# Kernel tuning notes

Measured on AMD Instinct MI355X. Metric: run time of the kernel, lower is better.

## Reference

```python
import jax, jax.numpy as jnp
import numpy as np

B, L, E, H = 64, 256, 1024, 16
HD = E // H
ROPE_BASE = 10000.0


def rope(x):
    # x: [B, H, L, HD]; torchtune-style interleaved RoPE along the seq axis
    Lx, D = x.shape[2], x.shape[3]
    inv_freq = 1.0 / (ROPE_BASE ** (jnp.arange(0, D, 2, dtype=jnp.float32) / D))
    ang = jnp.arange(Lx, dtype=jnp.float32)[:, None] * inv_freq[None, :]  # [L, D/2]
    cos, sin = jnp.cos(ang), jnp.sin(ang)
    x0, x1 = x[..., 0::2], x[..., 1::2]
    r0 = x0 * cos - x1 * sin
    r1 = x1 * cos + x0 * sin
    return jnp.stack([r0, r1], axis=-1).reshape(x.shape)


def setup_inputs() -> dict:
    key = jax.random.key(0)
    ks = jax.random.split(key, 6)
    s = 0.02
    return {
        "x": jax.random.normal(ks[0], (B, L, E), jnp.float32),
        "Wq": jax.random.normal(ks[1], (E, E), jnp.float32) * s,
        "bq": jnp.zeros((E,), jnp.float32),
        "Wk": jax.random.normal(ks[2], (E, E), jnp.float32) * s,
        "bk": jnp.zeros((E,), jnp.float32),
        "Wv": jax.random.normal(ks[3], (E, E), jnp.float32) * s,
        "bv": jnp.zeros((E,), jnp.float32),
        "Wo": jax.random.normal(ks[4], (E, E), jnp.float32) * s,
        "bo": jnp.zeros((E,), jnp.float32),
        "attention_mask": jnp.ones((B, L), bool),
    }


def reference(x, Wq, bq, Wk, bk, Wv, bv, Wo, bo, attention_mask):
    Bq, Lq, _ = x.shape
    # QKV projections (nn.Linear: y = x @ W.T + b), split heads -> [B, H, L, HD]
    q = (x @ Wq.T + bq).reshape(Bq, Lq, H, HD).transpose(0, 2, 1, 3)
    k = (x @ Wk.T + bk).reshape(Bq, Lq, H, HD).transpose(0, 2, 1, 3)
    v = (x @ Wv.T + bv).reshape(Bq, Lq, H, HD).transpose(0, 2, 1, 3)
    q = rope(q)
    k = rope(k)
    # combined causal + padding mask: [B, 1, Lq, Lq]
    causal = jnp.tril(jnp.ones((Lq, Lq), bool))
    mask = causal[None, None, :, :] & attention_mask[:, None, None, :]
    scale = 1.0 / np.sqrt(HD).astype(np.float32)
    scores = jnp.einsum('bhqd,bhkd->bhqk', q, k) * scale
    scores = jnp.where(mask, scores, jnp.finfo(scores.dtype).min)
    attn = jax.nn.softmax(scores, axis=-1)
    out = jnp.einsum('bhqk,bhkd->bhqd', attn, v)
    out = out.transpose(0, 2, 1, 3).reshape(Bq, Lq, E)
    return out @ Wo.T + bo
```

## Files before the change

kernel.cpp:

```cpp
#include <hip/hip_runtime.h>
#include <hip/hip_bf16.h>

typedef __attribute__((ext_vector_type(4))) float f32x4;
typedef __attribute__((ext_vector_type(8))) short s16x8;
typedef unsigned short ushort_t;

__device__ __forceinline__ ushort_t f2bf(float f) {
    union { float f; unsigned u; } v; v.f = f;
    unsigned r = v.u + 0x7fffu + ((v.u >> 16) & 1u);
    return (ushort_t)(r >> 16);
}

__device__ __forceinline__ void gload16(const ushort_t* g, ushort_t* l) {
    __builtin_amdgcn_global_load_lds(
        (const __attribute__((address_space(1))) unsigned int*)g,
        (__attribute__((address_space(3))) unsigned int*)l,
        16, 0, 0);
}

#define BAR()  asm volatile("s_barrier" ::: "memory")
#define LGK0() do { asm volatile("s_waitcnt lgkmcnt(0)" ::: "memory"); __builtin_amdgcn_sched_barrier(0); } while (0)
#define VMC(n) asm volatile("s_waitcnt vmcnt(" #n ")" ::: "memory")

__global__ void cvt_bf16(const float* __restrict__ in, ushort_t* __restrict__ out, int n8) {
    int i = blockIdx.x * blockDim.x + threadIdx.x;
    if (i >= n8) return;
    const float4* p = (const float4*)in;
    float4 a = p[2 * i], b = p[2 * i + 1];
    s16x8 v;
    v[0] = (short)f2bf(a.x); v[1] = (short)f2bf(a.y);
    v[2] = (short)f2bf(a.z); v[3] = (short)f2bf(a.w);
    v[4] = (short)f2bf(b.x); v[5] = (short)f2bf(b.y);
    v[6] = (short)f2bf(b.z); v[7] = (short)f2bf(b.w);
    *(s16x8*)(out + (size_t)i * 8) = v;
}

__global__ void rope_tab_k(float* __restrict__ cosT, float* __restrict__ sinT) {
    int i = blockIdx.x * blockDim.x + threadIdx.x;
    int l = i >> 5, fi = i & 31;
    float inv = powf(10000.f, -2.f * (float)fi / 64.f);
    float ang = (float)l * inv;
    cosT[i] = cosf(ang);
    sinT[i] = sinf(ang);
}


__device__ __forceinline__ void stage32(const ushort_t* __restrict__ src,
                                        ushort_t* chunk, int tid, int kk) {
#pragma unroll
    for (int j = 0; j < 2; ++j) {
        int row = (tid >> 2) + j * 128;
        int gslot = (tid & 3) ^ ((row >> 1) & 3);
        gload16(src + (size_t)row * 1024 + kk + gslot * 8,
                chunk + (size_t)tid * 8 + (size_t)j * 4096);
    }
}

__device__ __forceinline__ s16x8 rdA32(const ushort_t* chunk, int wm, int m, int lane) {
    int row = wm * 128 + m * 16 + (lane & 15);
    int slot = (lane >> 4) ^ ((row >> 1) & 3);
    return *(const s16x8*)&chunk[row * 32 + (slot << 3)];
}
__device__ __forceinline__ s16x8 rdB32(const ushort_t* chunk, int wn, int n, int lane) {
    int row = wn * 64 + n * 16 + (lane & 15);
    int slot = (lane >> 4) ^ ((row >> 1) & 3);
    return *(const s16x8*)&chunk[row * 32 + (slot << 3)];
}

template <int MODE>
__global__ __launch_bounds__(512, 2) void gemm256(const ushort_t* __restrict__ A,
                                                  const ushort_t* __restrict__ Wt,
                                                  const float* __restrict__ bz0,
                                                  const float* __restrict__ bz1,
                                                  const float* __restrict__ bz2,
                                                  ushort_t* __restrict__ o0,
                                                  ushort_t* __restrict__ o1,
                                                  ushort_t* __restrict__ o2,
                                                  float* __restrict__ of,
                                                  const float* __restrict__ cosT,
                                                  const float* __restrict__ sinT,
                                                  int ntn) {
    __shared__ ushort_t lds[4][2][8192];

    const int nwg = 64 * ntn;
    const int orig = blockIdx.x;
    const int wg = (orig % 8) * (nwg / 8) + orig / 8;
    const int tn = wg % ntn, tm = wg / ntn;

    const int tid = threadIdx.x, lane = tid & 63, wid = tid >> 6;
    const int wm = wid >> 2, wn = wid & 3;

    f32x4 acc[8][4];
#pragma unroll
    for (int i = 0; i < 8; ++i)
#pragma unroll
        for (int j = 0; j < 4; ++j) acc[i][j] = (f32x4){0.f, 0.f, 0.f, 0.f};

    const ushort_t* Abase = A + (size_t)(tm * 256) * 1024;
    const ushort_t* Bbase = Wt + (size_t)(tn * 256) * 1024;

#pragma unroll
    for (int p = 0; p < 3; ++p) {
        stage32(Abase, &lds[p][0][0], tid, p * 32);
        stage32(Bbase, &lds[p][1][0], tid, p * 32);
    }

#pragma unroll 1
    for (int u = 0; u < 32; ++u) {
        const ushort_t* cA = &lds[u & 3][0][0];
        const ushort_t* cB = &lds[u & 3][1][0];
        ushort_t* sA = &lds[(u + 3) & 3][0][0];
        ushort_t* sB = &lds[(u + 3) & 3][1][0];
        const int kt = (u + 3 < 32 ? u + 3 : 31) * 32;
        s16x8 b_[4], a_[8];

        VMC(8);
        BAR();
        stage32(Abase, sA, tid, kt);
        stage32(Bbase, sB, tid, kt);
#pragma unroll
        for (int n = 0; n < 4; ++n) b_[n] = rdB32(cB, wn, n, lane);
#pragma unroll
        for (int m = 0; m < 8; ++m) a_[m] = rdA32(cA, wm, m, lane);
        LGK0();
        __builtin_amdgcn_s_setprio(1);
#pragma unroll
        for (int m = 0; m < 8; ++m)
#pragma unroll
            for (int n = 0; n < 4; ++n)
                acc[m][n] = __builtin_amdgcn_mfma_f32_16x16x32_bf16(a_[m], b_[n], acc[m][n], 0, 0, 0);
        __builtin_amdgcn_s_setprio(0);
    }
    VMC(0);

    const int rb0 = tm * 256 + wm * 128 + ((lane >> 4) << 2);
    if (MODE == 0) {
        const int zz = (tn * 256) >> 10;
        const float* bias = (zz == 0) ? bz0 : (zz == 1) ? bz1 : bz2;
        ushort_t* outp = (zz == 0) ? o0 : (zz == 1) ? o1 : o2;
        const bool rope = (zz < 2);
        const int cb = (tn & 3) * 256 + wn * 64;
#pragma unroll
        for (int m = 0; m < 8; ++m) {
#pragma unroll
            for (int n = 0; n < 4; ++n) {
                int col = cb + n * 16 + (lane & 15);
                float bv_ = bias[col];
                int rb = rb0 + m * 16;
#pragma unroll
                for (int r = 0; r < 4; ++r) {
                    float v = acc[m][n][r] + bv_;
                    float res;
                    if (rope) {
                        int l = (rb + r) & 255;
                        int fi = (col & 63) >> 1;
                        float c = cosT[l * 32 + fi], s = sinT[l * 32 + fi];
                        float partner = __shfl_xor(v, 1);
                        res = (col & 1) ? (v * c + partner * s) : (v * c - partner * s);
                    } else {
                        res = v;
                    }
                    outp[(size_t)(rb + r) * 1024 + col] = f2bf(res);
                }
            }
        }
    } else {
        const int cb = wn * 64;
        const int cfull = tn * 256 + cb;
#pragma unroll
        for (int m = 0; m < 8; ++m) {
#pragma unroll
            for (int n = 0; n < 4; ++n) {
                int col = cfull + n * 16 + (lane & 15);
                float bv_ = bz0[col];
                int rb = rb0 + m * 16;
#pragma unroll
                for (int r = 0; r < 4; ++r)
                    of[(size_t)(rb + r) * 1024 + col] = acc[m][n][r] + bv_;
            }
        }
    }
}

__global__ __launch_bounds__(512) void attn_kernel(const ushort_t* __restrict__ qb,
                                                   const ushort_t* __restrict__ kb,
                                                   const ushort_t* __restrict__ vb,
                                                   ushort_t* __restrict__ ab) {
    __shared__ ushort_t Ks[256 * 72];
    __shared__ ushort_t Vt[64 * 264];
    __shared__ ushort_t Ps[8][16 * 264];
    const int bh = blockIdx.x, b = bh >> 4, h = bh & 15;
    const int tid = threadIdx.x, lane = tid & 63, wid = tid >> 6;
    const size_t base = (size_t)b * 256 * 1024 + (size_t)h * 64;

#pragma unroll
    for (int it = 0; it < 4; ++it) {
        int c = tid + it * 512;
        int row = c >> 3, seg = c & 7;
        *(s16x8*)&Ks[row * 72 + seg * 8] =
            *(const s16x8*)&kb[base + (size_t)row * 1024 + seg * 8];
    }
#pragma unroll
    for (int it = 0; it < 4; ++it) {
        int c = tid + it * 512;
        int k = c >> 3, seg = c & 7;
        s16x8 v8 = *(const s16x8*)&vb[base + (size_t)k * 1024 + seg * 8];
#pragma unroll
        for (int j = 0; j < 8; ++j)
            Vt[(seg * 8 + j) * 264 + k] = (ushort_t)v8[j];
    }
    __syncthreads();

#pragma unroll
    for (int ch = 0; ch < 2; ++ch) {
        const int q0 = wid * 32 + ch * 16;
        const int ntop = q0 >> 4;
        s16x8 aq0 = *(const s16x8*)&qb[base + (size_t)(q0 + (lane & 15)) * 1024 + ((lane >> 4) << 3)];
        s16x8 aq1 = *(const s16x8*)&qb[base + (size_t)(q0 + (lane & 15)) * 1024 + 32 + ((lane >> 4) << 3)];

        f32x4 sacc[16];
#pragma unroll
        for (int n = 0; n < 16; ++n) sacc[n] = (f32x4){0.f, 0.f, 0.f, 0.f};
#pragma unroll
        for (int n = 0; n < 16; ++n) {
            if (n <= ntop) {
                const int kr = (n * 16 + (lane & 15)) * 72 + ((lane >> 4) << 3);
                s16x8 b0 = *(const s16x8*)&Ks[kr];
                s16x8 b1 = *(const s16x8*)&Ks[kr + 32];
                sacc[n] = __builtin_amdgcn_mfma_f32_16x16x32_bf16(aq0, b0, sacc[n], 0, 0, 0);
                sacc[n] = __builtin_amdgcn_mfma_f32_16x16x32_bf16(aq1, b1, sacc[n], 0, 0, 0);
            }
        }

        float rinv[4];
#pragma unroll
        for (int r = 0; r < 4; ++r) {
            const int row = q0 + ((lane >> 4) << 2) + r;
            float m = -1e30f;
#pragma unroll
            for (int n = 0; n < 16; ++n) {
                int col = n * 16 + (lane & 15);
                float v = (col <= row) ? sacc[n][r] * 0.125f : -1e30f;
                sacc[n][r] = v;
                m = fmaxf(m, v);
            }
            m = fmaxf(m, __shfl_xor(m, 1));
            m = fmaxf(m, __shfl_xor(m, 2));
            m = fmaxf(m, __shfl_xor(m, 4));
            m = fmaxf(m, __shfl_xor(m, 8));
            float sum = 0.f;
#pragma unroll
            for (int n = 0; n < 16; ++n) {
                float p = __expf(sacc[n][r] - m);
                sacc[n][r] = p;
                sum += p;
            }
            sum += __shfl_xor(sum, 1);
            sum += __shfl_xor(sum, 2);
            sum += __shfl_xor(sum, 4);
            sum += __shfl_xor(sum, 8);
            rinv[r] = 1.f / sum;
#pragma unroll
            for (int n = 0; n < 16; ++n)
                Ps[wid][(((lane >> 4) << 2) + r) * 264 + n * 16 + (lane & 15)] = f2bf(sacc[n][r]);
        }
        __syncthreads();

        f32x4 oa[4];
#pragma unroll
        for (int dt = 0; dt < 4; ++dt) oa[dt] = (f32x4){0.f, 0.f, 0.f, 0.f};
        const int kstop = q0 >> 5;
#pragma unroll
        for (int ks = 0; ks < 8; ++ks) {
            if (ks <= kstop) {
                s16x8 pf = *(const s16x8*)&Ps[wid][(lane & 15) * 264 + ks * 32 + ((lane >> 4) << 3)];
#pragma unroll
                for (int dt = 0; dt < 4; ++dt) {
                    s16x8 vf = *(const s16x8*)&Vt[(dt * 16 + (lane & 15)) * 264 + ks * 32 + ((lane >> 4) << 3)];
                    oa[dt] = __builtin_amdgcn_mfma_f32_16x16x32_bf16(pf, vf, oa[dt], 0, 0, 0);
                }
            }
        }
#pragma unroll
        for (int dt = 0; dt < 4; ++dt) {
#pragma unroll
            for (int r = 0; r < 4; ++r) {
                int row = q0 + ((lane >> 4) << 2) + r;
                int col = h * 64 + dt * 16 + (lane & 15);
                ab[(size_t)(b * 256 + row) * 1024 + col] = f2bf(oa[dt][r] * rinv[r]);
            }
        }
        __syncthreads();
    }
}

extern "C" void kernel_launch(void* const* d_in, const int* in_sizes, int n_in,
                              void* d_out, int out_size, void* d_ws, size_t ws_size,
                              hipStream_t stream) {
    (void)in_sizes; (void)n_in; (void)out_size;
    const float* x  = (const float*)d_in[0];
    const float* Wq = (const float*)d_in[1];
    const float* bq = (const float*)d_in[2];
    const float* Wk = (const float*)d_in[3];
    const float* bk = (const float*)d_in[4];
    const float* Wv = (const float*)d_in[5];
    const float* bv = (const float*)d_in[6];
    const float* Wo = (const float*)d_in[7];
    const float* bo = (const float*)d_in[8];
    float* out = (float*)d_out;

    const size_t M = 16384, E = 1024;
    char* ws = (char*)d_ws;
    ushort_t* xb   = (ushort_t*)ws;
    ushort_t* wqkv = xb + M * E;
    ushort_t* wob  = wqkv + 3 * E * E;
    ushort_t* qb   = wob + E * E;
    ushort_t* kb   = qb + M * E;
    ushort_t* vb   = kb + M * E;
    float* cosT    = (float*)(vb + M * E);
    float* sinT    = cosT + 256 * 32;
    ushort_t* ab   = xb;

    size_t need = (4 * M * E + 4 * E * E) * sizeof(ushort_t) + 2 * 256 * 32 * sizeof(float);
    if (ws_size < need) return;

    cvt_bf16<<<8192, 256, 0, stream>>>(x, xb, (int)(M * E / 8));
    cvt_bf16<<<512, 256, 0, stream>>>(Wq, wqkv, (int)(E * E / 8));
    cvt_bf16<<<512, 256, 0, stream>>>(Wk, wqkv + E * E, (int)(E * E / 8));
    cvt_bf16<<<512, 256, 0, stream>>>(Wv, wqkv + 2 * E * E, (int)(E * E / 8));
    cvt_bf16<<<512, 256, 0, stream>>>(Wo, wob, (int)(E * E / 8));
    rope_tab_k<<<32, 256, 0, stream>>>(cosT, sinT);

    gemm256<0><<<768, 512, 0, stream>>>(xb, wqkv, bq, bk, bv, qb, kb, vb, nullptr,
                                        cosT, sinT, 12);
    attn_kernel<<<1024, 512, 0, stream>>>(qb, kb, vb, ab);
    gemm256<1><<<256, 512, 0, stream>>>(ab, wob, bo, nullptr, nullptr,
                                        nullptr, nullptr, nullptr, out, nullptr, nullptr, 4);
}
```

Baseline: 281.8 us.

## Shrink GEMM M-tile to 128 with double buffering, stream P tiles in attention

The projection GEMMs move from 256x256 tiles with a 4-stage LDS pipeline to 128x256 tiles with two buffers. Loads for the next stage are interleaved with two half-MFMA phases, and launch bounds allow higher occupancy. The attention kernel now writes P into a small per-wave 16x32 scratch inside the PV loop instead of a full 16x256 buffer, which shrinks LDS and drops block-wide barriers. The four weight conversions are merged into one launch. The shallower pipeline and a VMC(0)+barrier every iteration may expose memory latency. Per-wave reuse of the Ps scratch also has no intra-wave sync beyond wave lockstep.

```diff
diff --git a/kernel.cpp b/kernel.cpp
--- a/kernel.cpp
+++ b/kernel.cpp
@@ -35,6 +35,23 @@
     *(s16x8*)(out + (size_t)i * 8) = v;
 }
 
+__global__ void cvt_w4(const float* __restrict__ w0, const float* __restrict__ w1,
+                       const float* __restrict__ w2, const float* __restrict__ w3,
+                       ushort_t* __restrict__ out) {
+    const float* src = (blockIdx.y == 0) ? w0 : (blockIdx.y == 1) ? w1
+                     : (blockIdx.y == 2) ? w2 : w3;
+    ushort_t* dst = out + (size_t)blockIdx.y * 1024 * 1024;
+    int i = blockIdx.x * blockDim.x + threadIdx.x;
+    const float4* p = (const float4*)src;
+    float4 a = p[2 * i], b = p[2 * i + 1];
+    s16x8 v;
+    v[0] = (short)f2bf(a.x); v[1] = (short)f2bf(a.y);
+    v[2] = (short)f2bf(a.z); v[3] = (short)f2bf(a.w);
+    v[4] = (short)f2bf(b.x); v[5] = (short)f2bf(b.y);
+    v[6] = (short)f2bf(b.z); v[7] = (short)f2bf(b.w);
+    *(s16x8*)(dst + (size_t)i * 8) = v;
+}
+
 __global__ void rope_tab_k(float* __restrict__ cosT, float* __restrict__ sinT) {
     int i = blockIdx.x * blockDim.x + threadIdx.x;
     int l = i >> 5, fi = i & 31;
@@ -45,8 +62,14 @@
 }
 
 
-__device__ __forceinline__ void stage32(const ushort_t* __restrict__ src,
-                                        ushort_t* chunk, int tid, int kk) {
+__device__ __forceinline__ void stageA32(const ushort_t* __restrict__ src,
+                                         ushort_t* chunk, int tid, int kk) {
+    int row = tid >> 2;
+    int gslot = (tid & 3) ^ ((row >> 1) & 3);
+    gload16(src + (size_t)row * 1024 + kk + gslot * 8, chunk + (size_t)tid * 8);
+}
+__device__ __forceinline__ void stageB32(const ushort_t* __restrict__ src,
+                                         ushort_t* chunk, int tid, int kk) {
 #pragma unroll
     for (int j = 0; j < 2; ++j) {
         int row = (tid >> 2) + j * 128;
@@ -57,7 +80,7 @@
 }
 
 __device__ __forceinline__ s16x8 rdA32(const ushort_t* chunk, int wm, int m, int lane) {
-    int row = wm * 128 + m * 16 + (lane & 15);
+    int row = wm * 64 + m * 16 + (lane & 15);
     int slot = (lane >> 4) ^ ((row >> 1) & 3);
     return *(const s16x8*)&chunk[row * 32 + (slot << 3)];
 }
@@ -68,7 +91,7 @@
 }
 
 template <int MODE>
-__global__ __launch_bounds__(512, 2) void gemm256(const ushort_t* __restrict__ A,
+__global__ __launch_bounds__(512, 4) void gemm128(const ushort_t* __restrict__ A,
                                                   const ushort_t* __restrict__ Wt,
                                                   const float* __restrict__ bz0,
                                                   const float* __restrict__ bz1,
@@ -80,9 +103,9 @@
                                                   const float* __restrict__ cosT,
                                                   const float* __restrict__ sinT,
                                                   int ntn) {
-    __shared__ ushort_t lds[4][2][8192];
-
-    const int nwg = 64 * ntn;
+    __shared__ ushort_t lds[2][12288];
+
+    const int nwg = 128 * ntn;
     const int orig = blockIdx.x;
     const int wg = (orig % 8) * (nwg / 8) + orig / 8;
     const int tn = wg % ntn, tm = wg / ntn;
@@ -90,58 +113,67 @@
     const int tid = threadIdx.x, lane = tid & 63, wid = tid >> 6;
     const int wm = wid >> 2, wn = wid & 3;
 
-    f32x4 acc[8][4];
-#pragma unroll
-    for (int i = 0; i < 8; ++i)
+    f32x4 acc[4][4];
+#pragma unroll
+    for (int i = 0; i < 4; ++i)
 #pragma unroll
         for (int j = 0; j < 4; ++j) acc[i][j] = (f32x4){0.f, 0.f, 0.f, 0.f};
 
-    const ushort_t* Abase = A + (size_t)(tm * 256) * 1024;
+    const ushort_t* Abase = A + (size_t)(tm * 128) * 1024;
     const ushort_t* Bbase = Wt + (size_t)(tn * 256) * 1024;
 
-#pragma unroll
-    for (int p = 0; p < 3; ++p) {
-        stage32(Abase, &lds[p][0][0], tid, p * 32);
-        stage32(Bbase, &lds[p][1][0], tid, p * 32);
-    }
+    stageA32(Abase, &lds[0][0], tid, 0);
+    stageB32(Bbase, &lds[0][4096], tid, 0);
+    VMC(0);
+    BAR();
 
 #pragma unroll 1
     for (int u = 0; u < 32; ++u) {
-        const ushort_t* cA = &lds[u & 3][0][0];
-        const ushort_t* cB = &lds[u & 3][1][0];
-        ushort_t* sA = &lds[(u + 3) & 3][0][0];
-        ushort_t* sB = &lds[(u + 3) & 3][1][0];
-        const int kt = (u + 3 < 32 ? u + 3 : 31) * 32;
-        s16x8 b_[4], a_[8];
-
-        VMC(8);
-        BAR();
-        stage32(Abase, sA, tid, kt);
-        stage32(Bbase, sB, tid, kt);
+        const int cur = u & 1;
+        const ushort_t* cA = &lds[cur][0];
+        const ushort_t* cB = &lds[cur][4096];
+        ushort_t* nA = &lds[cur ^ 1][0];
+        ushort_t* nB = &lds[cur ^ 1][4096];
+        const int kt = (u + 1 < 32 ? u + 1 : 31) * 32;
+        s16x8 b_[4], a_[2], a2_[2];
+
 #pragma unroll
         for (int n = 0; n < 4; ++n) b_[n] = rdB32(cB, wn, n, lane);
-#pragma unroll
-        for (int m = 0; m < 8; ++m) a_[m] = rdA32(cA, wm, m, lane);
+        a_[0] = rdA32(cA, wm, 0, lane); a_[1] = rdA32(cA, wm, 1, lane);
+        stageA32(Abase, nA, tid, kt);
         LGK0();
         __builtin_amdgcn_s_setprio(1);
 #pragma unroll
-        for (int m = 0; m < 8; ++m)
+        for (int m = 0; m < 2; ++m)
 #pragma unroll
             for (int n = 0; n < 4; ++n)
                 acc[m][n] = __builtin_amdgcn_mfma_f32_16x16x32_bf16(a_[m], b_[n], acc[m][n], 0, 0, 0);
         __builtin_amdgcn_s_setprio(0);
-    }
-    VMC(0);
-
-    const int rb0 = tm * 256 + wm * 128 + ((lane >> 4) << 2);
+
+        a2_[0] = rdA32(cA, wm, 2, lane); a2_[1] = rdA32(cA, wm, 3, lane);
+        stageB32(Bbase, nB, tid, kt);
+        LGK0();
+        __builtin_amdgcn_s_setprio(1);
+#pragma unroll
+        for (int m = 0; m < 2; ++m)
+#pragma unroll
+            for (int n = 0; n < 4; ++n)
+                acc[m + 2][n] = __builtin_amdgcn_mfma_f32_16x16x32_bf16(a2_[m], b_[n], acc[m + 2][n], 0, 0, 0);
+        __builtin_amdgcn_s_setprio(0);
+
+        VMC(0);
+        BAR();
+    }
+
+    const int rb0 = tm * 128 + wm * 64 + ((lane >> 4) << 2);
     if (MODE == 0) {
-        const int zz = (tn * 256) >> 10;
+        const int zz = tn >> 2;
         const float* bias = (zz == 0) ? bz0 : (zz == 1) ? bz1 : bz2;
         ushort_t* outp = (zz == 0) ? o0 : (zz == 1) ? o1 : o2;
         const bool rope = (zz < 2);
         const int cb = (tn & 3) * 256 + wn * 64;
 #pragma unroll
-        for (int m = 0; m < 8; ++m) {
+        for (int m = 0; m < 4; ++m) {
 #pragma unroll
             for (int n = 0; n < 4; ++n) {
                 int col = cb + n * 16 + (lane & 15);
@@ -165,10 +197,9 @@
             }
         }
     } else {
-        const int cb = wn * 64;
-        const int cfull = tn * 256 + cb;
-#pragma unroll
-        for (int m = 0; m < 8; ++m) {
+        const int cfull = tn * 256 + wn * 64;
+#pragma unroll
+        for (int m = 0; m < 4; ++m) {
 #pragma unroll
             for (int n = 0; n < 4; ++n) {
                 int col = cfull + n * 16 + (lane & 15);
@@ -182,13 +213,13 @@
     }
 }
 
-__global__ __launch_bounds__(512) void attn_kernel(const ushort_t* __restrict__ qb,
-                                                   const ushort_t* __restrict__ kb,
-                                                   const ushort_t* __restrict__ vb,
-                                                   ushort_t* __restrict__ ab) {
+__global__ __launch_bounds__(512, 4) void attn_kernel(const ushort_t* __restrict__ qb,
+                                                      const ushort_t* __restrict__ kb,
+                                                      const ushort_t* __restrict__ vb,
+                                                      ushort_t* __restrict__ ab) {
     __shared__ ushort_t Ks[256 * 72];
     __shared__ ushort_t Vt[64 * 264];
-    __shared__ ushort_t Ps[8][16 * 264];
+    __shared__ ushort_t Ps[8][16 * 40];
     const int bh = blockIdx.x, b = bh >> 4, h = bh & 15;
     const int tid = threadIdx.x, lane = tid & 63, wid = tid >> 6;
     const size_t base = (size_t)b * 256 * 1024 + (size_t)h * 64;
@@ -260,11 +291,7 @@
             sum += __shfl_xor(sum, 4);
             sum += __shfl_xor(sum, 8);
             rinv[r] = 1.f / sum;
-#pragma unroll
-            for (int n = 0; n < 16; ++n)
-                Ps[wid][(((lane >> 4) << 2) + r) * 264 + n * 16 + (lane & 15)] = f2bf(sacc[n][r]);
-        }
-        __syncthreads();
+        }
 
         f32x4 oa[4];
 #pragma unroll
@@ -273,7 +300,15 @@
 #pragma unroll
         for (int ks = 0; ks < 8; ++ks) {
             if (ks <= kstop) {
-                s16x8 pf = *(const s16x8*)&Ps[wid][(lane & 15) * 264 + ks * 32 + ((lane >> 4) << 3)];
+#pragma unroll
+                for (int nl = 0; nl < 2; ++nl) {
+                    const int n = 2 * ks + nl;
+#pragma unroll
+                    for (int r = 0; r < 4; ++r)
+                        Ps[wid][(((lane >> 4) << 2) + r) * 40 + nl * 16 + (lane & 15)] =
+                            f2bf(sacc[n][r]);
+                }
+                s16x8 pf = *(const s16x8*)&Ps[wid][(lane & 15) * 40 + ((lane >> 4) << 3)];
 #pragma unroll
                 for (int dt = 0; dt < 4; ++dt) {
                     s16x8 vf = *(const s16x8*)&Vt[(dt * 16 + (lane & 15)) * 264 + ks * 32 + ((lane >> 4) << 3)];
@@ -290,7 +325,6 @@
                 ab[(size_t)(b * 256 + row) * 1024 + col] = f2bf(oa[dt][r] * rinv[r]);
             }
         }
-        __syncthreads();
     }
 }
 
@@ -325,15 +359,12 @@
     if (ws_size < need) return;
 
     cvt_bf16<<<8192, 256, 0, stream>>>(x, xb, (int)(M * E / 8));
-    cvt_bf16<<<512, 256, 0, stream>>>(Wq, wqkv, (int)(E * E / 8));
-    cvt_bf16<<<512, 256, 0, stream>>>(Wk, wqkv + E * E, (int)(E * E / 8));
-    cvt_bf16<<<512, 256, 0, stream>>>(Wv, wqkv + 2 * E * E, (int)(E * E / 8));
-    cvt_bf16<<<512, 256, 0, stream>>>(Wo, wob, (int)(E * E / 8));
+    cvt_w4<<<dim3(512, 4), 256, 0, stream>>>(Wq, Wk, Wv, Wo, wqkv);
     rope_tab_k<<<32, 256, 0, stream>>>(cosT, sinT);
 
-    gemm256<0><<<768, 512, 0, stream>>>(xb, wqkv, bq, bk, bv, qb, kb, vb, nullptr,
-                                        cosT, sinT, 12);
+    gemm128<0><<<1536, 512, 0, stream>>>(xb, wqkv, bq, bk, bv, qb, kb, vb, nullptr,
+                                         cosT, sinT, 12);
     attn_kernel<<<1024, 512, 0, stream>>>(qb, kb, vb, ab);
-    gemm256<1><<<256, 512, 0, stream>>>(ab, wob, bo, nullptr, nullptr,
+    gemm128<1><<<512, 512, 0, stream>>>(ab, wob, bo, nullptr, nullptr,
                                         nullptr, nullptr, nullptr, out, nullptr, nullptr, 4);
 }
```

New measurement: 239.4 us, median of 3. -15.0%, faster.
